# Optimization experiments

Hardware: AMD Instinct MI355X
Metric: run time of the kernel (lower is better)

## Reference

```python
import jax, jax.numpy as jnp
import numpy as np

N_USERS = 100_000
N_ITEMS = 50_000
N_NODES = N_USERS + N_ITEMS
D = 64
NUM_LAYERS = 3
N_INTER = 1_000_000  # interactions; symmetrized -> 2M directed edges
BATCH = 4096


def setup_inputs() -> dict:
    key = jax.random.key(0)
    k_u, k_i, k_r, k_c, k_uid, k_iid = jax.random.split(key, 6)
    user_embedding = jax.random.normal(k_u, (N_USERS, D), dtype=jnp.float32)
    item_embedding = jax.random.normal(k_i, (N_ITEMS, D), dtype=jnp.float32)

    # build symmetric normalized adjacency edges as in get_norm_adj_mat
    rng = np.random.default_rng(0)
    row = rng.integers(0, N_USERS, size=N_INTER)
    col = rng.integers(0, N_ITEMS, size=N_INTER) + N_USERS
    src = np.concatenate([row, col])
    dst = np.concatenate([col, row])
    deg = np.bincount(src, minlength=N_NODES).astype(np.float32)
    norm_deg = 1.0 / np.sqrt(np.where(deg == 0, 1.0, deg))
    edge_weight = (norm_deg[src] * norm_deg[dst]).astype(np.float32)
    edge_index = np.stack([src, dst]).astype(np.int64)

    user_id = jax.random.randint(k_uid, (BATCH,), 0, N_USERS)
    item_id = jax.random.randint(k_iid, (BATCH,), 0, N_ITEMS)
    return {
        "user_embedding": user_embedding,
        "item_embedding": item_embedding,
        "edge_weight": jnp.asarray(edge_weight),
        "edge_index": jnp.asarray(edge_index),
        "user_id": user_id,
        "item_id": item_id,
    }


def reference(user_embedding, item_embedding, edge_weight, edge_index, user_id, item_id):
    # ego embeddings: [N_NODES, D]
    x = jnp.concatenate([user_embedding, item_embedding], axis=0)
    src, dst = edge_index[0], edge_index[1]
    h = x
    acc = x  # running sum over layer outputs (incl. layer 0)
    for _ in range(NUM_LAYERS):
        # LightGCNConv: gather source, scale by edge weight, scatter-add to dest
        msg = h[src] * edge_weight[:, None]                       # [E, D]
        h = jax.ops.segment_sum(msg, dst, num_segments=N_NODES)   # [N, D]
        acc = acc + h
    final = acc / jnp.asarray(NUM_LAYERS + 1, dtype=x.dtype)      # mean over layers
    u_embed = final[:N_USERS][user_id]
    i_embed = final[N_USERS:][item_id]
    return (u_embed, i_embed)
```

## Files before the change

kernel.cpp:

```cpp
#include <hip/hip_runtime.h>

#define N_USERS 100000
#define N_NODES 150000
#define DIM 64
#define BATCH 4096
#define BSHIFT 9
#define BUCKET 512
#define NB 293
#define PAIRS_PER_BLK 2048
#define EDGES_PER_BLK (2 * PAIRS_PER_BLK)
#define CAPSHIFT 14
#define CAP (1 << CAPSHIFT)

typedef unsigned short bf16_t;

static __device__ __forceinline__ float bf2f(bf16_t h) {
    return __uint_as_float(((unsigned)h) << 16);
}
static __device__ __forceinline__ bf16_t f2bf(float f) {
    unsigned u = __float_as_uint(f);
    return (bf16_t)((u + 0x7FFFu + ((u >> 16) & 1u)) >> 16);
}

__global__ void __launch_bounds__(256)
lgcn_bin(const int* __restrict__ row, const int* __restrict__ col,
         int* __restrict__ cursor, int* __restrict__ binned, int EH) {
    __shared__ int h[4 * NB];
    __shared__ int sA[512], sB[512];
    __shared__ int gb[NB];
    __shared__ int lo[NB];
    __shared__ int lc[NB];
    __shared__ int2 stage[EDGES_PER_BLK];

    int tid = threadIdx.x;
    for (int i = tid; i < 4 * NB; i += 256) h[i] = 0;
    __syncthreads();
    int k = blockIdx.x;
    int e0 = k * PAIRS_PER_BLK;
    int e1 = min(EH, e0 + PAIRS_PER_BLK);
    int nq = (e1 - e0) >> 2;
    const int4* r4 = (const int4*)(row + e0);
    const int4* c4 = (const int4*)(col + e0);
    int wv = tid >> 6;
    int* hw = h + wv * NB;
    for (int q = tid; q < nq; q += 256) {
        int4 r = r4[q];
        int4 c = c4[q];
        atomicAdd(&hw[r.x >> BSHIFT], 1); atomicAdd(&hw[c.x >> BSHIFT], 1);
        atomicAdd(&hw[r.y >> BSHIFT], 1); atomicAdd(&hw[c.y >> BSHIFT], 1);
        atomicAdd(&hw[r.z >> BSHIFT], 1); atomicAdd(&hw[c.z >> BSHIFT], 1);
        atomicAdd(&hw[r.w >> BSHIFT], 1); atomicAdd(&hw[c.w >> BSHIFT], 1);
    }
    __syncthreads();
    for (int i = tid; i < 512; i += 256)
        sA[i] = (i < NB) ? (h[i] + h[NB + i] + h[2 * NB + i] + h[3 * NB + i]) : 0;
    __syncthreads();
    int* c_ = sA; int* n_ = sB;
    for (int off = 1; off < 512; off <<= 1) {
        for (int i = tid; i < 512; i += 256)
            n_[i] = (i >= off) ? c_[i] + c_[i - off] : c_[i];
        __syncthreads();
        int* t = c_; c_ = n_; n_ = t;
    }
    for (int i = tid; i < NB; i += 256) {
        int tot = h[i] + h[NB + i] + h[2 * NB + i] + h[3 * NB + i];
        int excl = c_[i] - tot;
        lo[i] = excl;
        lc[i] = excl;
        int base = i << CAPSHIFT;
        if (tot) base += atomicAdd(&cursor[i], tot);
        gb[i] = base;
    }
    __syncthreads();
    for (int q = tid; q < nq; q += 256) {
        int4 r = r4[q];
        int4 c = c4[q];
        int rr[4] = { r.x, r.y, r.z, r.w };
        int cc[4] = { c.x, c.y, c.z, c.w };
#pragma unroll
        for (int j = 0; j < 4; ++j) {
            int b1 = cc[j] >> BSHIFT;
            int p1 = atomicAdd(&lc[b1], 1);
            stage[p1] = make_int2(gb[b1] + (p1 - lo[b1]),
                                  ((cc[j] & (BUCKET - 1)) << 18) | rr[j]);
            int b2 = rr[j] >> BSHIFT;
            int p2 = atomicAdd(&lc[b2], 1);
            stage[p2] = make_int2(gb[b2] + (p2 - lo[b2]),
                                  ((rr[j] & (BUCKET - 1)) << 18) | cc[j]);
        }
    }
    __syncthreads();
    int totAll = 2 * (e1 - e0);
    for (int s = tid; s < totAll; s += 256) {
        int2 v = stage[s];
        binned[v.x] = v.y;
    }
}

__global__ void __launch_bounds__(BUCKET)
lgcn_build_csr(const int* __restrict__ cursor, const int* __restrict__ binned,
               int4* __restrict__ nodeinfo, int* __restrict__ packed) {
    __shared__ int hist[BUCKET], sA[BUCKET], sB[BUCKET], cur[BUCKET];
    int b = blockIdx.x;
    int tid = threadIdx.x;
    hist[tid] = 0;
    __syncthreads();
    int e0 = b << CAPSHIFT;
    int e1 = e0 + cursor[b];
    for (int j = e0 + tid; j < e1; j += BUCKET)
        atomicAdd(&hist[binned[j] >> 18], 1);
    __syncthreads();
    int deg = hist[tid];
    int degp = (deg + 3) & ~3;
    sA[tid] = degp;
    __syncthreads();
    int* c_ = sA; int* n_ = sB;
    for (int off = 1; off < BUCKET; off <<= 1) {
        n_[tid] = (tid >= off) ? c_[tid] + c_[tid - off] : c_[tid];
        __syncthreads();
        int* t = c_; c_ = n_; n_ = t;
    }
    int start = e0 + (c_[tid] - degp);
    cur[tid] = start;
    int node = (b << BSHIFT) + tid;
    if (node < N_NODES) {
        float da = (deg == 0) ? 1.0f : (float)deg;
        float sq = sqrtf(da);
        int4 ni;
        ni.x = start;
        ni.y = deg;
        ni.z = __float_as_int(1.0f / sq);
        ni.w = __float_as_int(sq);
        nodeinfo[node] = ni;
    }
    __syncthreads();
    for (int j = e0 + tid; j < e1; j += BUCKET) {
        int w = binned[j];
        int pos = atomicAdd(&cur[w >> 18], 1);
        packed[pos] = w & 0x3FFFF;
    }
    for (int kk = deg; kk < degp; ++kk)
        packed[start + kk] = N_NODES;
}


__global__ void lgcn_init_g0(const float* __restrict__ ue, const float* __restrict__ ie,
                             const int4* __restrict__ nodeinfo,
                             bf16_t* __restrict__ g0, bf16_t* __restrict__ g1) {
    int t = blockIdx.x * blockDim.x + threadIdx.x;
    const int nT = N_NODES * (DIM / 4);
    if (t >= nT) {
        if (t < nT + 16)
            ((ushort4*)g0)[nT + (t - nT)] = make_ushort4(0, 0, 0, 0);
        else if (t < nT + 32)
            ((ushort4*)g1)[nT + (t - nT - 16)] = make_ushort4(0, 0, 0, 0);
        return;
    }
    int n = t >> 4;
    const int nU = N_USERS * (DIM / 4);
    float4 x = (t < nU) ? ((const float4*)ue)[t] : ((const float4*)ie)[t - nU];
    float nm = __int_as_float(nodeinfo[n].z);
    ushort4 o;
    o.x = f2bf(x.x * nm); o.y = f2bf(x.y * nm);
    o.z = f2bf(x.z * nm); o.w = f2bf(x.w * nm);
    ((ushort4*)g0)[t] = o;
}

static __device__ __forceinline__ float4
gather_sum(const bf16_t* __restrict__ g, const int* __restrict__ packed,
           int start, int deg, int grp, int c) {
    float4 acc = make_float4(0.f, 0.f, 0.f, 0.f);
    for (int o = 4 * grp; o < deg; o += 16) {
        int4 e4 = *(const int4*)(packed + start + o);
        ushort4 v0 = ((const ushort4*)(g + (size_t)e4.x * DIM))[c];
        ushort4 v1 = ((const ushort4*)(g + (size_t)e4.y * DIM))[c];
        ushort4 v2 = ((const ushort4*)(g + (size_t)e4.z * DIM))[c];
        ushort4 v3 = ((const ushort4*)(g + (size_t)e4.w * DIM))[c];
        acc.x += bf2f(v0.x); acc.y += bf2f(v0.y);
        acc.z += bf2f(v0.z); acc.w += bf2f(v0.w);
        acc.x += bf2f(v1.x); acc.y += bf2f(v1.y);
        acc.z += bf2f(v1.z); acc.w += bf2f(v1.w);
        acc.x += bf2f(v2.x); acc.y += bf2f(v2.y);
        acc.z += bf2f(v2.z); acc.w += bf2f(v2.w);
        acc.x += bf2f(v3.x); acc.y += bf2f(v3.y);
        acc.z += bf2f(v3.z); acc.w += bf2f(v3.w);
    }
    return acc;
}

__global__ void __launch_bounds__(256)
lgcn_pull(const bf16_t* __restrict__ g, const int4* __restrict__ nodeinfo,
          const int* __restrict__ packed, bf16_t* __restrict__ gn) {
    int n = blockIdx.x * 4 + (threadIdx.x >> 6);
    if (n >= N_NODES) return;
    int lane = threadIdx.x & 63;
    int grp = lane >> 4;
    int c = lane & 15;
    int4 ni = nodeinfo[n];
    float4 acc = gather_sum(g, packed, ni.x, ni.y, grp, c);
#pragma unroll
    for (int off = 16; off < 64; off <<= 1) {
        acc.x += __shfl_xor(acc.x, off, 64);
        acc.y += __shfl_xor(acc.y, off, 64);
        acc.z += __shfl_xor(acc.z, off, 64);
        acc.w += __shfl_xor(acc.w, off, 64);
    }
    if (lane < 16) {
        float nm = __int_as_float(ni.z);
        float s2 = nm * nm;
        ushort4 o;
        o.x = f2bf(acc.x * s2); o.y = f2bf(acc.y * s2);
        o.z = f2bf(acc.z * s2); o.w = f2bf(acc.w * s2);
        ((ushort4*)(gn + (size_t)n * DIM))[c] = o;
    }
}

__global__ void __launch_bounds__(256)
lgcn_final(const float* __restrict__ ue, const float* __restrict__ ie,
           const bf16_t* __restrict__ g1, const bf16_t* __restrict__ g2,
           const int4* __restrict__ nodeinfo, const int* __restrict__ packed,
           const int* __restrict__ uid, const int* __restrict__ iid,
           float* __restrict__ out) {
    int slot = blockIdx.x * 4 + (threadIdx.x >> 6);
    if (slot >= 2 * BATCH) return;
    int lane = threadIdx.x & 63;
    int grp = lane >> 4;
    int c = lane & 15;
    int isItem = slot >= BATCH;
    int b = isItem ? (slot - BATCH) : slot;
    int node = isItem ? (N_USERS + iid[b]) : uid[b];
    int4 ni = nodeinfo[node];
    float4 acc = gather_sum(g2, packed, ni.x, ni.y, grp, c);
#pragma unroll
    for (int off = 16; off < 64; off <<= 1) {
        acc.x += __shfl_xor(acc.x, off, 64);
        acc.y += __shfl_xor(acc.y, off, 64);
        acc.z += __shfl_xor(acc.z, off, 64);
        acc.w += __shfl_xor(acc.w, off, 64);
    }
    if (lane < 16) {
        const float* xb = isItem ? (ie + (size_t)(node - N_USERS) * DIM)
                                 : (ue + (size_t)node * DIM);
        float4 x = ((const float4*)xb)[c];
        ushort4 a1 = ((const ushort4*)(g1 + (size_t)node * DIM))[c];
        ushort4 a2 = ((const ushort4*)(g2 + (size_t)node * DIM))[c];
        float rn = __int_as_float(ni.w);
        float nm = __int_as_float(ni.z);
        float4 r;
        r.x = 0.25f * (x.x + rn * (bf2f(a1.x) + bf2f(a2.x)) + nm * acc.x);
        r.y = 0.25f * (x.y + rn * (bf2f(a1.y) + bf2f(a2.y)) + nm * acc.y);
        r.z = 0.25f * (x.z + rn * (bf2f(a1.z) + bf2f(a2.z)) + nm * acc.z);
        r.w = 0.25f * (x.w + rn * (bf2f(a1.w) + bf2f(a2.w)) + nm * acc.w);
        ((float4*)(out + (size_t)slot * DIM))[c] = r;
    }
}


extern "C" void kernel_launch(void* const* d_in, const int* in_sizes, int n_in,
                              void* d_out, int out_size, void* d_ws, size_t ws_size,
                              hipStream_t stream) {
    const float* ue  = (const float*)d_in[0];
    const float* ie  = (const float*)d_in[1];
    const int*   ei  = (const int*)d_in[3];
    const int*   uid = (const int*)d_in[4];
    const int*   iid = (const int*)d_in[5];
    float* out = (float*)d_out;

    const int E  = in_sizes[2];
    const int EH = E / 2;
    const int* row = ei;
    const int* col = ei + E;

    const int NB1 = (EH + PAIRS_PER_BLK - 1) / PAIRS_PER_BLK;

    char* p = (char*)d_ws;
    size_t off = 0;
    auto carve = [&](size_t bytes) -> char* {
        char* r = p + off;
        off += (bytes + 255) & ~(size_t)255;
        return r;
    };
    const size_t nodeBf16 = (size_t)(N_NODES + 1) * DIM * sizeof(bf16_t);
    bf16_t* gA       = (bf16_t*)carve(nodeBf16);
    bf16_t* gB       = (bf16_t*)carve(nodeBf16);
    int4*   nodeinfo = (int4*)carve((size_t)N_NODES * sizeof(int4));
    int*    cursor   = (int*)carve((size_t)NB * sizeof(int));
    int*    binned   = (int*)carve((size_t)NB * CAP * sizeof(int));
    int*    packed   = (int*)carve((size_t)NB * CAP * sizeof(int));
    (void)ws_size;

    hipMemsetAsync(cursor, 0, (size_t)NB * sizeof(int), stream);
    lgcn_bin<<<NB1, 256, 0, stream>>>(row, col, cursor, binned, EH);
    lgcn_build_csr<<<NB, BUCKET, 0, stream>>>(cursor, binned, nodeinfo, packed);

    lgcn_init_g0<<<(N_NODES * (DIM / 4) + 32 + 255) / 256, 256, 0, stream>>>(
        ue, ie, nodeinfo, gA, gB);

    const int pullGrid = (N_NODES + 3) / 4;
    lgcn_pull<<<pullGrid, 256, 0, stream>>>(gA, nodeinfo, packed, gB);
    lgcn_pull<<<pullGrid, 256, 0, stream>>>(gB, nodeinfo, packed, gA);
    lgcn_final<<<(2 * BATCH + 3) / 4, 256, 0, stream>>>(
        ue, ie, gB, gA, nodeinfo, packed, uid, iid, out);
}
```

Before: 239.3 us.

## Halve bucket size and fuse ego-embedding init into CSR build kernel

Bucket width drops from 512 to 256 nodes, doubling the number of buckets and CSR-build blocks and halving the per-bucket capacity. The separate init_g0 kernel is removed. Each build_csr block now scales and converts its own nodes' embeddings to bf16 using its shared-memory degree histogram and also writes the zero sentinel row. This saves one kernel launch and the nodeinfo reread, but grows the bin kernel's prefix scan to 1024 entries and raises the risk that a bucket overflows its smaller capacity.

```diff
diff --git a/kernel.cpp b/kernel.cpp
--- a/kernel.cpp
+++ b/kernel.cpp
@@ -4,12 +4,12 @@
 #define N_NODES 150000
 #define DIM 64
 #define BATCH 4096
-#define BSHIFT 9
-#define BUCKET 512
-#define NB 293
+#define BSHIFT 8
+#define BUCKET 256
+#define NB 586
 #define PAIRS_PER_BLK 2048
 #define EDGES_PER_BLK (2 * PAIRS_PER_BLK)
-#define CAPSHIFT 14
+#define CAPSHIFT 13
 #define CAP (1 << CAPSHIFT)
 
 typedef unsigned short bf16_t;
@@ -26,7 +26,7 @@
 lgcn_bin(const int* __restrict__ row, const int* __restrict__ col,
          int* __restrict__ cursor, int* __restrict__ binned, int EH) {
     __shared__ int h[4 * NB];
-    __shared__ int sA[512], sB[512];
+    __shared__ int sA[1024], sB[1024];
     __shared__ int gb[NB];
     __shared__ int lo[NB];
     __shared__ int lc[NB];
@@ -52,12 +52,12 @@
         atomicAdd(&hw[r.w >> BSHIFT], 1); atomicAdd(&hw[c.w >> BSHIFT], 1);
     }
     __syncthreads();
-    for (int i = tid; i < 512; i += 256)
+    for (int i = tid; i < 1024; i += 256)
         sA[i] = (i < NB) ? (h[i] + h[NB + i] + h[2 * NB + i] + h[3 * NB + i]) : 0;
     __syncthreads();
     int* c_ = sA; int* n_ = sB;
-    for (int off = 1; off < 512; off <<= 1) {
-        for (int i = tid; i < 512; i += 256)
+    for (int off = 1; off < 1024; off <<= 1) {
+        for (int i = tid; i < 1024; i += 256)
             n_[i] = (i >= off) ? c_[i] + c_[i - off] : c_[i];
         __syncthreads();
         int* t = c_; c_ = n_; n_ = t;
@@ -99,7 +99,9 @@
 
 __global__ void __launch_bounds__(BUCKET)
 lgcn_build_csr(const int* __restrict__ cursor, const int* __restrict__ binned,
-               int4* __restrict__ nodeinfo, int* __restrict__ packed) {
+               int4* __restrict__ nodeinfo, int* __restrict__ packed,
+               const float* __restrict__ ue, const float* __restrict__ ie,
+               bf16_t* __restrict__ g0, bf16_t* __restrict__ gz) {
     __shared__ int hist[BUCKET], sA[BUCKET], sB[BUCKET], cur[BUCKET];
     int b = blockIdx.x;
     int tid = threadIdx.x;
@@ -141,30 +143,32 @@
     }
     for (int kk = deg; kk < degp; ++kk)
         packed[start + kk] = N_NODES;
-}
-
-
-__global__ void lgcn_init_g0(const float* __restrict__ ue, const float* __restrict__ ie,
-                             const int4* __restrict__ nodeinfo,
-                             bf16_t* __restrict__ g0, bf16_t* __restrict__ g1) {
-    int t = blockIdx.x * blockDim.x + threadIdx.x;
-    const int nT = N_NODES * (DIM / 4);
-    if (t >= nT) {
-        if (t < nT + 16)
-            ((ushort4*)g0)[nT + (t - nT)] = make_ushort4(0, 0, 0, 0);
-        else if (t < nT + 32)
-            ((ushort4*)g1)[nT + (t - nT - 16)] = make_ushort4(0, 0, 0, 0);
-        return;
-    }
-    int n = t >> 4;
-    const int nU = N_USERS * (DIM / 4);
-    float4 x = (t < nU) ? ((const float4*)ue)[t] : ((const float4*)ie)[t - nU];
-    float nm = __int_as_float(nodeinfo[n].z);
-    ushort4 o;
-    o.x = f2bf(x.x * nm); o.y = f2bf(x.y * nm);
-    o.z = f2bf(x.z * nm); o.w = f2bf(x.w * nm);
-    ((ushort4*)g0)[t] = o;
-}
+    const int nodeBase = b << BSHIFT;
+#pragma unroll
+    for (int kq = 0; kq < 16; ++kq) {
+        int slot = kq * BUCKET + tid;
+        int nl = slot >> 4;
+        int cc = slot & 15;
+        int n = nodeBase + nl;
+        if (n > N_NODES) continue;
+        if (n == N_NODES) {
+            ((ushort4*)(g0 + (size_t)N_NODES * DIM))[cc] = make_ushort4(0, 0, 0, 0);
+            ((ushort4*)(gz + (size_t)N_NODES * DIM))[cc] = make_ushort4(0, 0, 0, 0);
+            continue;
+        }
+        int dg = hist[nl];
+        float da = (dg == 0) ? 1.0f : (float)dg;
+        float nm = 1.0f / sqrtf(da);
+        float4 x = (n < N_USERS)
+                 ? ((const float4*)ue)[(size_t)n * (DIM / 4) + cc]
+                 : ((const float4*)ie)[(size_t)(n - N_USERS) * (DIM / 4) + cc];
+        ushort4 o;
+        o.x = f2bf(x.x * nm); o.y = f2bf(x.y * nm);
+        o.z = f2bf(x.z * nm); o.w = f2bf(x.w * nm);
+        ((ushort4*)(g0 + (size_t)n * DIM))[cc] = o;
+    }
+}
+
 
 static __device__ __forceinline__ float4
 gather_sum(const bf16_t* __restrict__ g, const int* __restrict__ packed,
@@ -291,10 +295,8 @@
 
     hipMemsetAsync(cursor, 0, (size_t)NB * sizeof(int), stream);
     lgcn_bin<<<NB1, 256, 0, stream>>>(row, col, cursor, binned, EH);
-    lgcn_build_csr<<<NB, BUCKET, 0, stream>>>(cursor, binned, nodeinfo, packed);
-
-    lgcn_init_g0<<<(N_NODES * (DIM / 4) + 32 + 255) / 256, 256, 0, stream>>>(
-        ue, ie, nodeinfo, gA, gB);
+    lgcn_build_csr<<<NB, BUCKET, 0, stream>>>(cursor, binned, nodeinfo, packed,
+                                              ue, ie, gA, gB);
 
     const int pullGrid = (N_NODES + 3) / 4;
     lgcn_pull<<<pullGrid, 256, 0, stream>>>(gA, nodeinfo, packed, gB);
```

Result: slower. 255.3 us (+6.7%).
